# Kernel optimization log

Measured on AMD Instinct MI355X. Metric: run time of the kernel, lower is better.

The kernel has to match this reference:

```python
import jax, jax.numpy as jnp
import numpy as np

D, H, CTX, FFN, KS = 512, 8, 128, 2048, 31
B, S = 4, 4096
EPS = 1e-5

def _ln(x, g, b):
    m = jnp.mean(x, -1, keepdims=True)
    v = jnp.mean((x - m) ** 2, -1, keepdims=True)
    return (x - m) * jax.lax.rsqrt(v + EPS) * g + b

def _ffn(x, g, b, w1, b1, w2, b2):
    h = jax.nn.gelu(_ln(x, g, b) @ w1 + b1, approximate=False)
    return h @ w2 + b2

def _local_attn(x, wq, bq, wk, bk, wv, bv, wo, bo, rel_bias):
    Bz, Sz, Dz = x.shape
    Hd = Dz // H
    def proj(w, bias):
        return (x @ w + bias).reshape(Bz, Sz, H, Hd).transpose(0, 2, 1, 3)
    q, k, v = proj(wq, bq), proj(wk, bk), proj(wv, bv)
    nb = Sz // CTX
    def win(t):  # gather 3 neighboring blocks per query block -> [B,H,nb,3*CTX,Hd]
        tp = jnp.pad(t, ((0, 0), (0, 0), (CTX, CTX), (0, 0)))
        tb = tp.reshape(Bz, H, nb + 2, CTX, Hd)
        return jnp.concatenate([tb[:, :, :-2], tb[:, :, 1:-1], tb[:, :, 2:]], axis=3)
    kw, vw = win(k), win(v)
    qb = q.reshape(Bz, H, nb, CTX, Hd)
    scores = jnp.einsum('bhnqd,bhnkd->bhnqk', qb, kw) * (Hd ** -0.5)
    qi = jnp.arange(CTX)[:, None]
    kj = jnp.arange(3 * CTX)[None, :]
    rel = kj - CTX - qi  # [CTX, 3*CTX], relative position j - i
    scores = scores + rel_bias[:, jnp.clip(rel + CTX, 0, 2 * CTX)][None, :, None]
    j_glob = jnp.arange(nb)[:, None, None] * CTX - CTX + kj[None]  # [nb,1,3*CTX]
    valid = (jnp.abs(rel) <= CTX)[None] & (j_glob >= 0) & (j_glob < Sz)  # [nb,CTX,3*CTX]
    scores = jnp.where(valid[None, None], scores, -jnp.inf)
    w = jax.nn.softmax(scores, axis=-1)
    out = jnp.einsum('bhnqk,bhnkd->bhnqd', w, vw).reshape(Bz, H, Sz, Hd)
    out = out.transpose(0, 2, 1, 3).reshape(Bz, Sz, Dz)
    return out @ wo + bo

def _conv_mod(x, g, b, pw1_w, pw1_b, dw_w, dw_b, bn_g, bn_b, bn_m, bn_v, pw2_w, pw2_b):
    h = _ln(x, g, b) @ pw1_w + pw1_b  # [B,S,2D]
    a, gate = jnp.split(h, 2, axis=-1)
    h = a * jax.nn.sigmoid(gate)  # GLU
    hc = h.transpose(0, 2, 1)  # [B,D,S]
    hc = jax.lax.conv_general_dilated(
        hc, dw_w, (1,), [(KS // 2, KS // 2)],
        feature_group_count=D, dimension_numbers=('NCH', 'OIH', 'NCH')) + dw_b[None, :, None]
    hc = (hc - bn_m[None, :, None]) * jax.lax.rsqrt(bn_v[None, :, None] + EPS) * bn_g[None, :, None] + bn_b[None, :, None]
    hc = hc * jax.nn.sigmoid(hc)  # SiLU
    return hc.transpose(0, 2, 1) @ pw2_w + pw2_b

def setup_inputs() -> dict:
    key = jax.random.key(0)
    ks = iter(jax.random.split(key, 40))
    def w(*shape, s=0.02):
        return jax.random.normal(next(ks), shape, dtype=jnp.float32) * s
    d = {}
    d['x'] = jax.random.normal(next(ks), (B, S, D), dtype=jnp.float32)
    for p in ('ff1', 'ff2'):
        d[p + '_ln_g'] = jnp.ones((D,)); d[p + '_ln_b'] = jnp.zeros((D,))
        d[p + '_w1'] = w(D, FFN); d[p + '_b1'] = jnp.zeros((FFN,))
        d[p + '_w2'] = w(FFN, D); d[p + '_b2'] = jnp.zeros((D,))
    d['attn_ln_g'] = jnp.ones((D,)); d['attn_ln_b'] = jnp.zeros((D,))
    for p in ('wq', 'wk', 'wv', 'wo'):
        d[p] = w(D, D)
    for p in ('bq', 'bk', 'bv', 'bo'):
        d[p] = jnp.zeros((D,))
    d['rel_bias'] = w(H, 2 * CTX + 1)
    d['conv_ln_g'] = jnp.ones((D,)); d['conv_ln_b'] = jnp.zeros((D,))
    d['pw1_w'] = w(D, 2 * D); d['pw1_b'] = jnp.zeros((2 * D,))
    d['dw_w'] = w(D, 1, KS); d['dw_b'] = jnp.zeros((D,))
    d['bn_g'] = jnp.ones((D,)); d['bn_b'] = jnp.zeros((D,))
    d['bn_m'] = jnp.zeros((D,)); d['bn_v'] = jnp.ones((D,))
    d['pw2_w'] = w(D, D); d['pw2_b'] = jnp.zeros((D,))
    d['fin_ln_g'] = jnp.ones((D,)); d['fin_ln_b'] = jnp.zeros((D,))
    return d

def reference(x, ff1_ln_g, ff1_ln_b, ff1_w1, ff1_b1, ff1_w2, ff1_b2,
              ff2_ln_g, ff2_ln_b, ff2_w1, ff2_b1, ff2_w2, ff2_b2,
              attn_ln_g, attn_ln_b, wq, wk, wv, wo, bq, bk, bv, bo, rel_bias,
              conv_ln_g, conv_ln_b, pw1_w, pw1_b, dw_w, dw_b,
              bn_g, bn_b, bn_m, bn_v, pw2_w, pw2_b, fin_ln_g, fin_ln_b):
    x = x + 0.5 * _ffn(x, ff1_ln_g, ff1_ln_b, ff1_w1, ff1_b1, ff1_w2, ff1_b2)
    x = x + _local_attn(_ln(x, attn_ln_g, attn_ln_b), wq, bq, wk, bk, wv, bv, wo, bo, rel_bias)
    x = x + _conv_mod(x, conv_ln_g, conv_ln_b, pw1_w, pw1_b, dw_w, dw_b,
                      bn_g, bn_b, bn_m, bn_v, pw2_w, pw2_b)
    x = x + 0.5 * _ffn(x, ff2_ln_g, ff2_ln_b, ff2_w1, ff2_b1, ff2_w2, ff2_b2)
    return _ln(x, fin_ln_g, fin_ln_b)
```

## Files before the change

kernel.cpp:

```cpp
#include <hip/hip_runtime.h>
#include <hip/hip_bf16.h>
#include <math.h>


using bf16 = __hip_bfloat16;
typedef __bf16 bf16x8_t __attribute__((ext_vector_type(8)));
typedef float f32x4_t __attribute__((ext_vector_type(4)));

static __device__ __forceinline__ float bf2f(bf16 v) { return __bfloat162float(v); }
static __device__ __forceinline__ bf16 f2bf(float v) { return __float2bfloat16(v); }

#define GLOAD_LDS16(g, l)                                                            \
    __builtin_amdgcn_global_load_lds((const __attribute__((address_space(1))) void*)(g), \
                                     (__attribute__((address_space(3))) void*)(l), 16, 0, 0)

struct WSrcs { const float* s[10]; };
__global__ __launch_bounds__(256) void k_wconv(WSrcs srcs, bf16* __restrict__ wc) {
    const int start[11] = {0, 1024, 2048, 3072, 4096, 4352, 4608, 4864, 5120, 5632, 5888};
    const int Ks[10]    = {512, 2048, 512, 2048, 512, 512, 512, 512, 512, 512};
    const int Ns[10]    = {2048, 512, 2048, 512, 512, 512, 512, 512, 1024, 512};
    const int doff[10]  = {0, 1048576, 2097152, 3145728, 4194304, 4456448, 4718592, 4980736, 5242880, 5767168};
    int id = blockIdx.x, seg = 0;
#pragma unroll
    for (int i = 1; i < 10; ++i) seg += (id >= start[i]);
    int lid = id - start[seg];
    int K = Ks[seg], N = Ns[seg];
    int nbx = N >> 5;
    int bx = lid % nbx, by = lid / nbx;
    int nb = bx * 32, kb = by * 32;
    const float* in = srcs.s[seg];
    bf16* out = wc + doff[seg];
    bool inter = (seg == 8);
    __shared__ float t[32][33];
    int c = threadIdx.x & 31, r0 = threadIdx.x >> 5;
#pragma unroll
    for (int i = 0; i < 4; ++i)
        t[r0 + i * 8][c] = in[(size_t)(kb + r0 + i * 8) * N + nb + c];
    __syncthreads();
#pragma unroll
    for (int i = 0; i < 4; ++i) {
        int n = nb + r0 + i * 8;
        int orow = inter ? ((n < 512) ? 2 * n : 2 * (n - 512) + 1) : n;
        out[(size_t)orow * K + kb + c] = f2bf(t[c][r0 + i * 8]);
    }
}

template <bool BF16OUT>
__global__ __launch_bounds__(256) void k_ln(const float* __restrict__ x, const float* __restrict__ g,
                                            const float* __restrict__ b, void* __restrict__ outp) {
    int row = blockIdx.x * 4 + (threadIdx.x >> 6), t = threadIdx.x & 63;
    const float* xr = x + (size_t)row * 512 + t * 8;
    float4 v0 = *(const float4*)xr;
    float4 v1 = *(const float4*)(xr + 4);
    float vals[8] = {v0.x, v0.y, v0.z, v0.w, v1.x, v1.y, v1.z, v1.w};
    float s = 0.f, ss = 0.f;
#pragma unroll
    for (int j = 0; j < 8; ++j) { s += vals[j]; ss += vals[j] * vals[j]; }
#pragma unroll
    for (int o = 32; o > 0; o >>= 1) { s += __shfl_xor(s, o, 64); ss += __shfl_xor(ss, o, 64); }
    float mean = s * (1.0f / 512.0f);
    float var  = ss * (1.0f / 512.0f) - mean * mean;
    float r = rsqrtf(var + 1e-5f);
    float4 g0 = *(const float4*)(g + t * 8);
    float4 g1 = *(const float4*)(g + t * 8 + 4);
    float4 b0 = *(const float4*)(b + t * 8);
    float4 b1 = *(const float4*)(b + t * 8 + 4);
    float gv[8] = {g0.x, g0.y, g0.z, g0.w, g1.x, g1.y, g1.z, g1.w};
    float bv[8] = {b0.x, b0.y, b0.z, b0.w, b1.x, b1.y, b1.z, b1.w};
    float ov[8];
#pragma unroll
    for (int j = 0; j < 8; ++j) ov[j] = (vals[j] - mean) * r * gv[j] + bv[j];
    if (BF16OUT) {
        union { uint4 u; bf16 h[8]; } oo;
#pragma unroll
        for (int j = 0; j < 8; ++j) oo.h[j] = f2bf(ov[j]);
        *(uint4*)((bf16*)outp + (size_t)row * 512 + t * 8) = oo.u;
    } else {
        float* op = (float*)outp + (size_t)row * 512 + t * 8;
        *(float4*)op = make_float4(ov[0], ov[1], ov[2], ov[3]);
        *(float4*)(op + 4) = make_float4(ov[4], ov[5], ov[6], ov[7]);
    }
}

template <int MODE, int TN>
__global__ __launch_bounds__(256) void k_gemm(const bf16* __restrict__ A, const bf16* __restrict__ Bt,
                                              const float* __restrict__ bias, void* __restrict__ outp,
                                              int M, int N, int K, float scale,
                                              const float* __restrict__ b2, const float* __restrict__ b3,
                                              const float* __restrict__ resid, int nbx) {
    constexpr int TM = 128;
    constexpr int NT = TN / 32;
    __shared__ __align__(16) bf16 sm[2][(TM + TN) * 32];
    int id = blockIdx.x;
    int xcd = id & 7, slot = id >> 3;
    int nbyg = (gridDim.x / nbx) >> 3;
    int bxi = slot % nbx;
    int byi = slot / nbx + xcd * nbyg;
    int bn = bxi * TN, bm = byi * TM;
    int tid = threadIdx.x, w = tid >> 6, l = tid & 63;
    int l15 = l & 15, quad = l >> 4;
    int wm = (w >> 1) * 64, wn = (w & 1) * (TN / 2);
    f32x4_t acc[4][NT] = {};
    const int brows = TN / 4;
    const bf16* ag = A + (size_t)(bm + w * 32 + (l >> 2)) * K + (l & 3) * 8;
    const bf16* bg = Bt + (size_t)(bn + w * brows + (l >> 2)) * K + (l & 3) * 8;

    auto stage = [&](int buf, int k0) {
        bf16* asl = sm[buf] + w * 32 * 32;
        bf16* bsl = sm[buf] + TM * 32 + w * brows * 32;
#pragma unroll
        for (int j = 0; j < 2; ++j)
            GLOAD_LDS16(ag + (size_t)j * 16 * K + k0, asl + j * 16 * 32);
#pragma unroll
        for (int j = 0; j < TN / 64; ++j)
            GLOAD_LDS16(bg + (size_t)j * 16 * K + k0, bsl + j * 16 * 32);
    };
    auto compute = [&](int buf) {
        bf16x8_t af[4], bfr[NT];
#pragma unroll
        for (int tm = 0; tm < 4; ++tm)
            af[tm] = *(const bf16x8_t*)(sm[buf] + (wm + tm * 16 + l15) * 32 + quad * 8);
#pragma unroll
        for (int tn = 0; tn < NT; ++tn)
            bfr[tn] = *(const bf16x8_t*)(sm[buf] + TM * 32 + (wn + tn * 16 + l15) * 32 + quad * 8);
#pragma unroll
        for (int tm = 0; tm < 4; ++tm)
#pragma unroll
            for (int tn = 0; tn < NT; ++tn)
                acc[tm][tn] = __builtin_amdgcn_mfma_f32_16x16x32_bf16(af[tm], bfr[tn], acc[tm][tn], 0, 0, 0);
    };

    const int nt = K >> 5;
    stage(0, 0);
    int cur = 0;
    for (int t = 0; t < nt; ++t) {
        __syncthreads();
        if (t + 1 < nt) stage(cur ^ 1, (t + 1) * 32);
        compute(cur);
        cur ^= 1;
    }
    __syncthreads();
    float* tb = (float*)(&sm[0][0]) + w * 576;
#pragma unroll
    for (int tm = 0; tm < 4; ++tm)
#pragma unroll
        for (int cp = 0; cp < NT / 2; ++cp) {
#pragma unroll
            for (int j = 0; j < 2; ++j)
#pragma unroll
                for (int r = 0; r < 4; ++r)
                    tb[(quad * 4 + r) * 36 + j * 16 + l15] = acc[tm][2 * cp + j][r];
            int lr = l >> 2, lc = (l & 3) * 8;
            float v[8];
#pragma unroll
            for (int i = 0; i < 8; ++i) v[i] = tb[lr * 36 + lc + i];
            int gr = bm + wm + tm * 16 + lr;
            int gc = bn + wn + cp * 32 + lc;
            if (MODE == 0 || MODE == 1) {
                union { uint4 u; bf16 h[8]; } oo;
#pragma unroll
                for (int i = 0; i < 8; ++i) {
                    float vv = v[i] + bias[gc + i];
                    if (MODE == 1) {
                        float z = vv * (1.5957691f + 0.07135481f * vv * vv);
                        vv = vv / (1.f + __expf(-z));
                    }
                    oo.h[i] = f2bf(vv);
                }
                *(uint4*)((bf16*)outp + (size_t)gr * N + gc) = oo.u;
            } else if (MODE == 2) {
                size_t ix = (size_t)gr * N + gc;
                float4 r0 = *(const float4*)(resid + ix);
                float4 r1 = *(const float4*)(resid + ix + 4);
                float rr[8] = {r0.x, r0.y, r0.z, r0.w, r1.x, r1.y, r1.z, r1.w};
                float o[8];
#pragma unroll
                for (int i = 0; i < 8; ++i) o[i] = rr[i] + scale * (v[i] + bias[gc + i]);
                *(float4*)((float*)outp + ix) = make_float4(o[0], o[1], o[2], o[3]);
                *(float4*)((float*)outp + ix + 4) = make_float4(o[4], o[5], o[6], o[7]);
            } else if (MODE == 3) {
                const float* bp = (gc < 512) ? bias : (gc < 1024 ? b2 : b3);
                int cc = gc & 511;
                union { uint4 u; bf16 h[8]; } oo;
#pragma unroll
                for (int i = 0; i < 8; ++i) oo.h[i] = f2bf(v[i] + bp[cc + i]);
                bf16* ob = (bf16*)outp + (size_t)(gc >> 9) * 8388608;
                *(uint4*)(ob + (size_t)gr * 512 + cc) = oo.u;
            } else {
                union { ushort4 u; bf16 h[4]; } oo;
#pragma unroll
                for (int p = 0; p < 4; ++p) {
                    int ic = gc + 2 * p;
                    float a = v[2 * p] + bias[ic >> 1];
                    float gt = v[2 * p + 1] + bias[(ic >> 1) + 512];
                    oo.h[p] = f2bf(a / (1.f + __expf(-gt)));
                }
                *(ushort4*)((bf16*)outp + (size_t)gr * (N >> 1) + (gc >> 1)) = oo.u;
            }
        }
}

__global__ __launch_bounds__(256) void k_attn(const bf16* __restrict__ q, const bf16* __restrict__ k,
                                              const bf16* __restrict__ v, const float* __restrict__ rel_bias,
                                              bf16* __restrict__ out) {
    __shared__ __align__(16) bf16 Ks[64][72];
    __shared__ __align__(16) bf16 Vt[64][72];
    __shared__ __align__(16) bf16 Pb[4][32][72];
    __shared__ float relb2[512];
    int blk = blockIdx.x;
    int n = blk & 31, h = (blk >> 5) & 7, b = blk >> 8;
    int tid = threadIdx.x, w = tid >> 6, lane = tid & 63;
    int l15 = lane & 15, quad = lane >> 4;
    for (int i = tid; i < 512; i += 256) {
        int rel = i - 255;
        relb2[i] = (rel >= -128 && rel <= 128) ? rel_bias[h * 257 + rel + 128] : -INFINITY;
    }
    bf16x8_t qf[2][2];
#pragma unroll
    for (int qt = 0; qt < 2; ++qt)
#pragma unroll
        for (int ks = 0; ks < 2; ++ks) {
            const bf16* qg = q + (size_t)(b * 4096 + n * 128 + w * 32 + qt * 16 + l15) * 512
                               + h * 64 + ks * 32 + quad * 8;
            bf16x8_t f = *(const bf16x8_t*)qg;
#pragma unroll
            for (int j = 0; j < 8; ++j) f[j] = (__bf16)(0.125f * (float)f[j]);
            qf[qt][ks] = f;
        }
    float m_run[2][4], l_run[2][4];
#pragma unroll
    for (int qt = 0; qt < 2; ++qt)
#pragma unroll
        for (int r = 0; r < 4; ++r) { m_run[qt][r] = -1e30f; l_run[qt][r] = 0.f; }
    f32x4_t Oacc[2][4] = {};
    int kv0 = n * 128 - 128;
    int lo = (n == 0) ? 2 : 0;
    int hi = (n == 31) ? 4 : 6;
    int tbase = l15 + 127 - w * 32 - quad * 4;
    int krow = tid >> 3, kcol = (tid & 7) * 8;
    int vkey = tid >> 2, vc0 = (tid & 3) * 16;
    uint4 kr0, kr1;
    union { uint4 u[2]; bf16 hh[16]; } vr;
    auto loadKV = [&](int kst) {
        const bf16* kg = k + (size_t)(b * 4096 + kst + krow) * 512 + h * 64 + kcol;
        kr0 = *(const uint4*)kg;
        kr1 = *(const uint4*)(kg + (size_t)32 * 512);
        const bf16* vg = v + (size_t)(b * 4096 + kst + vkey) * 512 + h * 64 + vc0;
        vr.u[0] = *(const uint4*)vg;
        vr.u[1] = *(const uint4*)(vg + 8);
    };
    loadKV(kv0 + lo * 64);
    for (int ch = lo; ch < hi; ++ch) {
        __syncthreads();
        *(uint4*)&Ks[krow][kcol] = kr0;
        *(uint4*)&Ks[krow + 32][kcol] = kr1;
#pragma unroll
        for (int j = 0; j < 16; ++j) Vt[vc0 + j][vkey] = vr.hh[j];
        if (ch + 1 < hi) loadKV(kv0 + (ch + 1) * 64);
        __syncthreads();
        float sc[2][4][4];
        __builtin_amdgcn_s_setprio(1);
#pragma unroll
        for (int qt = 0; qt < 2; ++qt)
#pragma unroll
            for (int nt = 0; nt < 4; ++nt) {
                f32x4_t a = {};
#pragma unroll
                for (int ks = 0; ks < 2; ++ks) {
                    bf16x8_t kf = *(const bf16x8_t*)&Ks[nt * 16 + l15][ks * 32 + quad * 8];
                    a = __builtin_amdgcn_mfma_f32_16x16x32_bf16(qf[qt][ks], kf, a, 0, 0, 0);
                }
#pragma unroll
                for (int r = 0; r < 4; ++r) sc[qt][nt][r] = a[r];
            }
        __builtin_amdgcn_s_setprio(0);
        {
            int tb0 = tbase + ch * 64;
#pragma unroll
            for (int qt = 0; qt < 2; ++qt)
#pragma unroll
                for (int nt = 0; nt < 4; ++nt)
#pragma unroll
                    for (int r = 0; r < 4; ++r)
                        sc[qt][nt][r] += relb2[tb0 + nt * 16 - qt * 16 - r];
        }
        float mx[2][4];
        int need = 0;
#pragma unroll
        for (int qt = 0; qt < 2; ++qt)
#pragma unroll
            for (int r = 0; r < 4; ++r) {
                float m3 = fmaxf(fmaxf(sc[qt][0][r], sc[qt][1][r]), fmaxf(sc[qt][2][r], sc[qt][3][r]));
#pragma unroll
                for (int mk = 1; mk <= 8; mk <<= 1) m3 = fmaxf(m3, __shfl_xor(m3, mk, 64));
                mx[qt][r] = m3;
                need |= (m3 > m_run[qt][r] + 8.f) ? 1 : 0;
            }
        bool slow = __any(need);
        float al[2][4];
#pragma unroll
        for (int qt = 0; qt < 2; ++qt)
#pragma unroll
            for (int r = 0; r < 4; ++r) {
                float mn = slow ? fmaxf(m_run[qt][r], mx[qt][r]) : m_run[qt][r];
                float ps = 0.f;
#pragma unroll
                for (int nt = 0; nt < 4; ++nt) {
                    float p = __expf(sc[qt][nt][r] - mn);
                    sc[qt][nt][r] = p;
                    ps += p;
                }
#pragma unroll
                for (int mk = 1; mk <= 8; mk <<= 1) ps += __shfl_xor(ps, mk, 64);
                if (slow) {
                    float a = __expf(m_run[qt][r] - mn);
                    l_run[qt][r] = l_run[qt][r] * a + ps;
                    m_run[qt][r] = mn;
                    al[qt][r] = a;
                } else {
                    l_run[qt][r] += ps;
                }
            }
#pragma unroll
        for (int qt = 0; qt < 2; ++qt)
#pragma unroll
            for (int nt = 0; nt < 4; ++nt)
#pragma unroll
                for (int r = 0; r < 4; ++r)
                    Pb[w][qt * 16 + quad * 4 + r][nt * 16 + l15] = f2bf(sc[qt][nt][r]);
#pragma unroll
        for (int qt = 0; qt < 2; ++qt) {
            if (slow) {
#pragma unroll
                for (int dt = 0; dt < 4; ++dt)
#pragma unroll
                    for (int r = 0; r < 4; ++r)
                        Oacc[qt][dt][r] *= al[qt][r];
            }
            bf16x8_t pf[2];
#pragma unroll
            for (int ks = 0; ks < 2; ++ks)
                pf[ks] = *(const bf16x8_t*)&Pb[w][qt * 16 + l15][ks * 32 + quad * 8];
            __builtin_amdgcn_s_setprio(1);
#pragma unroll
            for (int dt = 0; dt < 4; ++dt) {
                f32x4_t a = Oacc[qt][dt];
#pragma unroll
                for (int ks = 0; ks < 2; ++ks) {
                    bf16x8_t vf = *(const bf16x8_t*)&Vt[dt * 16 + l15][ks * 32 + quad * 8];
                    a = __builtin_amdgcn_mfma_f32_16x16x32_bf16(pf[ks], vf, a, 0, 0, 0);
                }
                Oacc[qt][dt] = a;
            }
            __builtin_amdgcn_s_setprio(0);
        }
    }
#pragma unroll
    for (int qt = 0; qt < 2; ++qt)
#pragma unroll
        for (int r = 0; r < 4; ++r) {
            float inv = 1.f / l_run[qt][r];
            int row = n * 128 + w * 32 + qt * 16 + quad * 4 + r;
#pragma unroll
            for (int dt = 0; dt < 4; ++dt)
                out[(size_t)(b * 4096 + row) * 512 + h * 64 + dt * 16 + l15] = f2bf(Oacc[qt][dt][r] * inv);
        }
}

__global__ __launch_bounds__(256) void k_conv(const bf16* __restrict__ in, const float* __restrict__ w,
                                              const float* __restrict__ wb, const float* __restrict__ bg,
                                              const float* __restrict__ bb2, const float* __restrict__ bm,
                                              const float* __restrict__ bvv, bf16* __restrict__ out) {
    __shared__ float wl[64 * 31];
    int d0 = blockIdx.x * 64, s0 = blockIdx.y * 64, b = blockIdx.z;
    for (int i = threadIdx.x; i < 64 * 31; i += 256) wl[i] = w[d0 * 31 + i];
    __syncthreads();
    int dl = threadIdx.x & 63, chunk = threadIdx.x >> 6;
    int d = d0 + dl;
    int s00 = s0 + chunk * 16;
    float wr[31];
#pragma unroll
    for (int t = 0; t < 31; ++t) wr[t] = wl[dl * 31 + t];
    float xw[46];
    const bf16* base = in + (size_t)(b * 4096) * 512 + d;
#pragma unroll
    for (int i = 0; i < 46; ++i) {
        int s = s00 - 15 + i;
        xw[i] = (s >= 0 && s < 4096) ? bf2f(base[(size_t)s * 512]) : 0.f;
    }
    float scv = bg[d] * rsqrtf(bvv[d] + 1e-5f);
    float wbd = wb[d], bmd = bm[d], bbd = bb2[d];
    bf16* op = out + (size_t)(b * 4096 + s00) * 512 + d;
#pragma unroll
    for (int j = 0; j < 16; ++j) {
        float acc = 0.f;
#pragma unroll
        for (int t = 0; t < 31; ++t) acc += wr[t] * xw[j + t];
        acc += wbd;
        acc = (acc - bmd) * scv + bbd;
        acc = acc / (1.f + __expf(-acc));
        op[(size_t)j * 512] = f2bf(acc);
    }
}

extern "C" void kernel_launch(void* const* d_in, const int* in_sizes, int n_in,
                              void* d_out, int out_size, void* d_ws, size_t ws_size,
                              hipStream_t stream) {
    (void)in_sizes; (void)n_in; (void)out_size; (void)ws_size;
    const float* x = (const float*)d_in[0];
    char* ws = (char*)d_ws;
    float* xf   = (float*)ws;
    bf16* ln_bf = (bf16*)(ws + 33554432);
    bf16* h_bf  = (bf16*)(ws + 50331648);
    bf16* g_bf  = (bf16*)(ws + 117440512);
    bf16* t_bf  = (bf16*)(ws + 134217728);
    bf16* wc    = (bf16*)(ws + 150994944);
    bf16 *qb = h_bf;
    bf16* w_f11 = wc;
    bf16* w_f12 = wc + 1048576;
    bf16* w_f21 = wc + 2097152;
    bf16* w_f22 = wc + 3145728;
    bf16* w_q   = wc + 4194304;
    bf16* w_o   = wc + 4980736;
    bf16* w_p1  = wc + 5242880;
    bf16* w_p2  = wc + 5767168;

    WSrcs srcs;
    srcs.s[0] = (const float*)d_in[3];  srcs.s[1] = (const float*)d_in[5];
    srcs.s[2] = (const float*)d_in[9];  srcs.s[3] = (const float*)d_in[11];
    srcs.s[4] = (const float*)d_in[15]; srcs.s[5] = (const float*)d_in[16];
    srcs.s[6] = (const float*)d_in[17]; srcs.s[7] = (const float*)d_in[18];
    srcs.s[8] = (const float*)d_in[26]; srcs.s[9] = (const float*)d_in[34];
    k_wconv<<<5888, 256, 0, stream>>>(srcs, wc);

    k_ln<true><<<4096, 256, 0, stream>>>(x, (const float*)d_in[1], (const float*)d_in[2], ln_bf);
    k_gemm<1, 128><<<2048, 256, 0, stream>>>(ln_bf, w_f11, (const float*)d_in[4], h_bf, 16384, 2048, 512, 0.f, nullptr, nullptr, nullptr, 16);
    k_gemm<2, 128><<<512, 256, 0, stream>>>(h_bf, w_f12, (const float*)d_in[6], xf, 16384, 512, 2048, 0.5f, nullptr, nullptr, x, 4);
    k_ln<true><<<4096, 256, 0, stream>>>(xf, (const float*)d_in[13], (const float*)d_in[14], ln_bf);
    k_gemm<3, 128><<<1536, 256, 0, stream>>>(ln_bf, w_q, (const float*)d_in[19], qb, 16384, 1536, 512, 0.f,
                                             (const float*)d_in[20], (const float*)d_in[21], nullptr, 12);
    k_attn<<<1024, 256, 0, stream>>>(qb, qb + 8388608, qb + 16777216, (const float*)d_in[23], t_bf);
    k_gemm<2, 128><<<512, 256, 0, stream>>>(t_bf, w_o, (const float*)d_in[22], xf, 16384, 512, 512, 1.0f, nullptr, nullptr, xf, 4);
    k_ln<true><<<4096, 256, 0, stream>>>(xf, (const float*)d_in[24], (const float*)d_in[25], ln_bf);
    k_gemm<5, 128><<<1024, 256, 0, stream>>>(ln_bf, w_p1, (const float*)d_in[27], g_bf, 16384, 1024, 512, 0.f, nullptr, nullptr, nullptr, 8);
    k_conv<<<dim3(8, 64, 4), 256, 0, stream>>>(g_bf, (const float*)d_in[28], (const float*)d_in[29], (const float*)d_in[30],
                                               (const float*)d_in[31], (const float*)d_in[32], (const float*)d_in[33], t_bf);
    k_gemm<2, 128><<<512, 256, 0, stream>>>(t_bf, w_p2, (const float*)d_in[35], xf, 16384, 512, 512, 1.0f, nullptr, nullptr, xf, 4);
    k_ln<true><<<4096, 256, 0, stream>>>(xf, (const float*)d_in[7], (const float*)d_in[8], ln_bf);
    k_gemm<1, 128><<<2048, 256, 0, stream>>>(ln_bf, w_f21, (const float*)d_in[10], h_bf, 16384, 2048, 512, 0.f, nullptr, nullptr, nullptr, 16);
    k_gemm<2, 128><<<512, 256, 0, stream>>>(h_bf, w_f22, (const float*)d_in[12], xf, 16384, 512, 2048, 0.5f, nullptr, nullptr, xf, 4);
    k_ln<false><<<4096, 256, 0, stream>>>(xf, (const float*)d_in[36], (const float*)d_in[37], d_out);
}
```

Before: 598.3 us.

## Split attention block into 8 waves with 16 query rows each

The local-attention kernel now runs 512 threads per block (8 waves), each owning 16 query rows instead of 32, with the K/V chunk staging split across all threads. The aim is more waves in flight, fewer registers per wave (halved score and accumulator state), and more latency hiding, at the same total LDS footprint. The costs are that K/V fragment LDS reads per query row double and block-wide barriers now synchronize more waves.

```diff
diff --git a/kernel.cpp b/kernel.cpp
--- a/kernel.cpp
+++ b/kernel.cpp
@@ -200,171 +200,146 @@
         }
 }
 
-__global__ __launch_bounds__(256) void k_attn(const bf16* __restrict__ q, const bf16* __restrict__ k,
-                                              const bf16* __restrict__ v, const float* __restrict__ rel_bias,
-                                              bf16* __restrict__ out) {
+__global__ __launch_bounds__(512, 6) void k_attn(const bf16* __restrict__ q, const bf16* __restrict__ k,
+                                                 const bf16* __restrict__ v, const float* __restrict__ rel_bias,
+                                                 bf16* __restrict__ out) {
     __shared__ __align__(16) bf16 Ks[64][72];
     __shared__ __align__(16) bf16 Vt[64][72];
-    __shared__ __align__(16) bf16 Pb[4][32][72];
+    __shared__ __align__(16) bf16 Pb[8][16][72];
     __shared__ float relb2[512];
     int blk = blockIdx.x;
     int n = blk & 31, h = (blk >> 5) & 7, b = blk >> 8;
     int tid = threadIdx.x, w = tid >> 6, lane = tid & 63;
     int l15 = lane & 15, quad = lane >> 4;
-    for (int i = tid; i < 512; i += 256) {
-        int rel = i - 255;
-        relb2[i] = (rel >= -128 && rel <= 128) ? rel_bias[h * 257 + rel + 128] : -INFINITY;
-    }
-    bf16x8_t qf[2][2];
-#pragma unroll
-    for (int qt = 0; qt < 2; ++qt)
-#pragma unroll
-        for (int ks = 0; ks < 2; ++ks) {
-            const bf16* qg = q + (size_t)(b * 4096 + n * 128 + w * 32 + qt * 16 + l15) * 512
-                               + h * 64 + ks * 32 + quad * 8;
-            bf16x8_t f = *(const bf16x8_t*)qg;
-#pragma unroll
-            for (int j = 0; j < 8; ++j) f[j] = (__bf16)(0.125f * (float)f[j]);
-            qf[qt][ks] = f;
-        }
-    float m_run[2][4], l_run[2][4];
-#pragma unroll
-    for (int qt = 0; qt < 2; ++qt)
-#pragma unroll
-        for (int r = 0; r < 4; ++r) { m_run[qt][r] = -1e30f; l_run[qt][r] = 0.f; }
-    f32x4_t Oacc[2][4] = {};
+    {
+        int rel = tid - 255;
+        relb2[tid] = (rel >= -128 && rel <= 128) ? rel_bias[h * 257 + rel + 128] : -INFINITY;
+    }
+    bf16x8_t qf[2];
+#pragma unroll
+    for (int ks = 0; ks < 2; ++ks) {
+        const bf16* qg = q + (size_t)(b * 4096 + n * 128 + w * 16 + l15) * 512
+                           + h * 64 + ks * 32 + quad * 8;
+        bf16x8_t f = *(const bf16x8_t*)qg;
+#pragma unroll
+        for (int j = 0; j < 8; ++j) f[j] = (__bf16)(0.125f * (float)f[j]);
+        qf[ks] = f;
+    }
+    float m_run[4], l_run[4];
+#pragma unroll
+    for (int r = 0; r < 4; ++r) { m_run[r] = -1e30f; l_run[r] = 0.f; }
+    f32x4_t Oacc[4] = {};
     int kv0 = n * 128 - 128;
     int lo = (n == 0) ? 2 : 0;
     int hi = (n == 31) ? 4 : 6;
-    int tbase = l15 + 127 - w * 32 - quad * 4;
+    int tbase = l15 + 127 - w * 16 - quad * 4;
     int krow = tid >> 3, kcol = (tid & 7) * 8;
-    int vkey = tid >> 2, vc0 = (tid & 3) * 16;
-    uint4 kr0, kr1;
-    union { uint4 u[2]; bf16 hh[16]; } vr;
+    uint4 kr;
+    union { uint4 u; bf16 hh[8]; } vr;
     auto loadKV = [&](int kst) {
-        const bf16* kg = k + (size_t)(b * 4096 + kst + krow) * 512 + h * 64 + kcol;
-        kr0 = *(const uint4*)kg;
-        kr1 = *(const uint4*)(kg + (size_t)32 * 512);
-        const bf16* vg = v + (size_t)(b * 4096 + kst + vkey) * 512 + h * 64 + vc0;
-        vr.u[0] = *(const uint4*)vg;
-        vr.u[1] = *(const uint4*)(vg + 8);
+        kr = *(const uint4*)(k + (size_t)(b * 4096 + kst + krow) * 512 + h * 64 + kcol);
+        vr.u = *(const uint4*)(v + (size_t)(b * 4096 + kst + krow) * 512 + h * 64 + kcol);
     };
     loadKV(kv0 + lo * 64);
     for (int ch = lo; ch < hi; ++ch) {
         __syncthreads();
-        *(uint4*)&Ks[krow][kcol] = kr0;
-        *(uint4*)&Ks[krow + 32][kcol] = kr1;
-#pragma unroll
-        for (int j = 0; j < 16; ++j) Vt[vc0 + j][vkey] = vr.hh[j];
+        *(uint4*)&Ks[krow][kcol] = kr;
+#pragma unroll
+        for (int j = 0; j < 8; ++j) Vt[kcol + j][krow] = vr.hh[j];
         if (ch + 1 < hi) loadKV(kv0 + (ch + 1) * 64);
         __syncthreads();
-        float sc[2][4][4];
+        float sc[4][4];
         __builtin_amdgcn_s_setprio(1);
 #pragma unroll
-        for (int qt = 0; qt < 2; ++qt)
-#pragma unroll
-            for (int nt = 0; nt < 4; ++nt) {
-                f32x4_t a = {};
-#pragma unroll
-                for (int ks = 0; ks < 2; ++ks) {
-                    bf16x8_t kf = *(const bf16x8_t*)&Ks[nt * 16 + l15][ks * 32 + quad * 8];
-                    a = __builtin_amdgcn_mfma_f32_16x16x32_bf16(qf[qt][ks], kf, a, 0, 0, 0);
-                }
-#pragma unroll
-                for (int r = 0; r < 4; ++r) sc[qt][nt][r] = a[r];
+        for (int nt = 0; nt < 4; ++nt) {
+            f32x4_t a = {};
+#pragma unroll
+            for (int ks = 0; ks < 2; ++ks) {
+                bf16x8_t kf = *(const bf16x8_t*)&Ks[nt * 16 + l15][ks * 32 + quad * 8];
+                a = __builtin_amdgcn_mfma_f32_16x16x32_bf16(qf[ks], kf, a, 0, 0, 0);
             }
+#pragma unroll
+            for (int r = 0; r < 4; ++r) sc[nt][r] = a[r];
+        }
         __builtin_amdgcn_s_setprio(0);
         {
             int tb0 = tbase + ch * 64;
 #pragma unroll
-            for (int qt = 0; qt < 2; ++qt)
-#pragma unroll
-                for (int nt = 0; nt < 4; ++nt)
-#pragma unroll
-                    for (int r = 0; r < 4; ++r)
-                        sc[qt][nt][r] += relb2[tb0 + nt * 16 - qt * 16 - r];
-        }
-        float mx[2][4];
+            for (int nt = 0; nt < 4; ++nt)
+#pragma unroll
+                for (int r = 0; r < 4; ++r)
+                    sc[nt][r] += relb2[tb0 + nt * 16 - r];
+        }
+        float mx[4];
         int need = 0;
 #pragma unroll
-        for (int qt = 0; qt < 2; ++qt)
-#pragma unroll
-            for (int r = 0; r < 4; ++r) {
-                float m3 = fmaxf(fmaxf(sc[qt][0][r], sc[qt][1][r]), fmaxf(sc[qt][2][r], sc[qt][3][r]));
-#pragma unroll
-                for (int mk = 1; mk <= 8; mk <<= 1) m3 = fmaxf(m3, __shfl_xor(m3, mk, 64));
-                mx[qt][r] = m3;
-                need |= (m3 > m_run[qt][r] + 8.f) ? 1 : 0;
+        for (int r = 0; r < 4; ++r) {
+            float m3 = fmaxf(fmaxf(sc[0][r], sc[1][r]), fmaxf(sc[2][r], sc[3][r]));
+#pragma unroll
+            for (int mk = 1; mk <= 8; mk <<= 1) m3 = fmaxf(m3, __shfl_xor(m3, mk, 64));
+            mx[r] = m3;
+            need |= (m3 > m_run[r] + 8.f) ? 1 : 0;
+        }
+        bool slow = __any(need);
+        float al[4];
+#pragma unroll
+        for (int r = 0; r < 4; ++r) {
+            float mn = slow ? fmaxf(m_run[r], mx[r]) : m_run[r];
+            float ps = 0.f;
+#pragma unroll
+            for (int nt = 0; nt < 4; ++nt) {
+                float p = __expf(sc[nt][r] - mn);
+                sc[nt][r] = p;
+                ps += p;
             }
-        bool slow = __any(need);
-        float al[2][4];
-#pragma unroll
-        for (int qt = 0; qt < 2; ++qt)
-#pragma unroll
-            for (int r = 0; r < 4; ++r) {
-                float mn = slow ? fmaxf(m_run[qt][r], mx[qt][r]) : m_run[qt][r];
-                float ps = 0.f;
-#pragma unroll
-                for (int nt = 0; nt < 4; ++nt) {
-                    float p = __expf(sc[qt][nt][r] - mn);
-                    sc[qt][nt][r] = p;
-                    ps += p;
-                }
-#pragma unroll
-                for (int mk = 1; mk <= 8; mk <<= 1) ps += __shfl_xor(ps, mk, 64);
-                if (slow) {
-                    float a = __expf(m_run[qt][r] - mn);
-                    l_run[qt][r] = l_run[qt][r] * a + ps;
-                    m_run[qt][r] = mn;
-                    al[qt][r] = a;
-                } else {
-                    l_run[qt][r] += ps;
-                }
+#pragma unroll
+            for (int mk = 1; mk <= 8; mk <<= 1) ps += __shfl_xor(ps, mk, 64);
+            if (slow) {
+                float a = __expf(m_run[r] - mn);
+                l_run[r] = l_run[r] * a + ps;
+                m_run[r] = mn;
+                al[r] = a;
+            } else {
+                l_run[r] += ps;
             }
-#pragma unroll
-        for (int qt = 0; qt < 2; ++qt)
-#pragma unroll
-            for (int nt = 0; nt < 4; ++nt)
+        }
+#pragma unroll
+        for (int nt = 0; nt < 4; ++nt)
+#pragma unroll
+            for (int r = 0; r < 4; ++r)
+                Pb[w][quad * 4 + r][nt * 16 + l15] = f2bf(sc[nt][r]);
+        if (slow) {
+#pragma unroll
+            for (int dt = 0; dt < 4; ++dt)
 #pragma unroll
                 for (int r = 0; r < 4; ++r)
-                    Pb[w][qt * 16 + quad * 4 + r][nt * 16 + l15] = f2bf(sc[qt][nt][r]);
-#pragma unroll
-        for (int qt = 0; qt < 2; ++qt) {
-            if (slow) {
-#pragma unroll
-                for (int dt = 0; dt < 4; ++dt)
-#pragma unroll
-                    for (int r = 0; r < 4; ++r)
-                        Oacc[qt][dt][r] *= al[qt][r];
+                    Oacc[dt][r] *= al[r];
+        }
+        bf16x8_t pf[2];
+#pragma unroll
+        for (int ks = 0; ks < 2; ++ks)
+            pf[ks] = *(const bf16x8_t*)&Pb[w][l15][ks * 32 + quad * 8];
+        __builtin_amdgcn_s_setprio(1);
+#pragma unroll
+        for (int dt = 0; dt < 4; ++dt) {
+            f32x4_t a = Oacc[dt];
+#pragma unroll
+            for (int ks = 0; ks < 2; ++ks) {
+                bf16x8_t vf = *(const bf16x8_t*)&Vt[dt * 16 + l15][ks * 32 + quad * 8];
+                a = __builtin_amdgcn_mfma_f32_16x16x32_bf16(pf[ks], vf, a, 0, 0, 0);
             }
-            bf16x8_t pf[2];
-#pragma unroll
-            for (int ks = 0; ks < 2; ++ks)
-                pf[ks] = *(const bf16x8_t*)&Pb[w][qt * 16 + l15][ks * 32 + quad * 8];
-            __builtin_amdgcn_s_setprio(1);
-#pragma unroll
-            for (int dt = 0; dt < 4; ++dt) {
-                f32x4_t a = Oacc[qt][dt];
-#pragma unroll
-                for (int ks = 0; ks < 2; ++ks) {
-                    bf16x8_t vf = *(const bf16x8_t*)&Vt[dt * 16 + l15][ks * 32 + quad * 8];
-                    a = __builtin_amdgcn_mfma_f32_16x16x32_bf16(pf[ks], vf, a, 0, 0, 0);
-                }
-                Oacc[qt][dt] = a;
-            }
-            __builtin_amdgcn_s_setprio(0);
-        }
-    }
-#pragma unroll
-    for (int qt = 0; qt < 2; ++qt)
-#pragma unroll
-        for (int r = 0; r < 4; ++r) {
-            float inv = 1.f / l_run[qt][r];
-            int row = n * 128 + w * 32 + qt * 16 + quad * 4 + r;
-#pragma unroll
-            for (int dt = 0; dt < 4; ++dt)
-                out[(size_t)(b * 4096 + row) * 512 + h * 64 + dt * 16 + l15] = f2bf(Oacc[qt][dt][r] * inv);
-        }
+            Oacc[dt] = a;
+        }
+        __builtin_amdgcn_s_setprio(0);
+    }
+#pragma unroll
+    for (int r = 0; r < 4; ++r) {
+        float inv = 1.f / l_run[r];
+        int row = n * 128 + w * 16 + quad * 4 + r;
+#pragma unroll
+        for (int dt = 0; dt < 4; ++dt)
+            out[(size_t)(b * 4096 + row) * 512 + h * 64 + dt * 16 + l15] = f2bf(Oacc[dt][r] * inv);
+    }
 }
 
 __global__ __launch_bounds__(256) void k_conv(const bf16* __restrict__ in, const float* __restrict__ w,
@@ -439,7 +414,7 @@
     k_ln<true><<<4096, 256, 0, stream>>>(xf, (const float*)d_in[13], (const float*)d_in[14], ln_bf);
     k_gemm<3, 128><<<1536, 256, 0, stream>>>(ln_bf, w_q, (const float*)d_in[19], qb, 16384, 1536, 512, 0.f,
                                              (const float*)d_in[20], (const float*)d_in[21], nullptr, 12);
-    k_attn<<<1024, 256, 0, stream>>>(qb, qb + 8388608, qb + 16777216, (const float*)d_in[23], t_bf);
+    k_attn<<<1024, 512, 0, stream>>>(qb, qb + 8388608, qb + 16777216, (const float*)d_in[23], t_bf);
     k_gemm<2, 128><<<512, 256, 0, stream>>>(t_bf, w_o, (const float*)d_in[22], xf, 16384, 512, 512, 1.0f, nullptr, nullptr, xf, 4);
     k_ln<true><<<4096, 256, 0, stream>>>(xf, (const float*)d_in[24], (const float*)d_in[25], ln_bf);
     k_gemm<5, 128><<<1024, 256, 0, stream>>>(ln_bf, w_p1, (const float*)d_in[27], g_bf, 16384, 1024, 512, 0.f, nullptr, nullptr, nullptr, 8);
```

Measured after the change: 612.3 us. 2.3% more time.
